# Kernel tuning notes

Hardware: AMD Instinct MI355X
Metric: run time of the kernel (lower is better)

The kernel has to match this reference:

```python
import jax, jax.numpy as jnp
import numpy as np
from jax import lax

W_SIZE = 11
SIGMA = 1.5

def _gaussian_window(w_size, sigma, channel):
    x = np.arange(w_size) - w_size // 2
    g = np.exp(-(x.astype(np.float64) ** 2) / (2.0 * sigma ** 2))
    g = g / g.sum()
    w2d = np.outer(g, g).astype(np.float32)  # [w, w]
    # depthwise kernel in OIHW with feature_group_count=channel: [C, 1, w, w]
    return jnp.asarray(np.broadcast_to(w2d, (channel, 1, w_size, w_size)))

def _dwconv(x, window, channel):
    return lax.conv_general_dilated(
        x, window, window_strides=(1, 1), padding='VALID',
        dimension_numbers=('NCHW', 'OIHW', 'NCHW'),
        feature_group_count=channel)

def setup_inputs() -> dict:
    key = jax.random.key(0)
    k1, k2 = jax.random.split(key)
    B, C, H, W = 16, 3, 512, 512
    y_pred = jax.random.uniform(k1, (B, C, H, W), dtype=jnp.float32)
    y_true = jax.random.uniform(k2, (B, C, H, W), dtype=jnp.float32)
    return {"y_pred": y_pred, "y_true": y_true}

def reference(y_pred, y_true):
    channel = y_pred.shape[1]
    L = jnp.max(y_pred) - jnp.min(y_pred)
    window = _gaussian_window(W_SIZE, SIGMA, channel)

    mu1 = _dwconv(y_pred, window, channel)
    mu2 = _dwconv(y_true, window, channel)
    mu1_sq = mu1 * mu1
    mu2_sq = mu2 * mu2
    mu1_mu2 = mu1 * mu2
    sigma1_sq = _dwconv(y_pred * y_pred, window, channel) - mu1_sq
    sigma2_sq = _dwconv(y_true * y_true, window, channel) - mu2_sq
    sigma12 = _dwconv(y_pred * y_true, window, channel) - mu1_mu2

    C1 = (0.01 * L) ** 2
    C2 = (0.03 * L) ** 2
    v1 = 2.0 * sigma12 + C2
    v2 = sigma1_sq + sigma2_sq + C2
    ssim_map = (2.0 * mu1_mu2 + C1) * v1 / ((mu1_sq + mu2_sq + C1) * v2)
    # size_average=True, full=False defaults
    return -jnp.mean(ssim_map)
```

## Files before the change

### kernel.cpp

```cpp
#include <hip/hip_runtime.h>
#include <math.h>

#define IMG   512
#define OUTD  502
#define NBC   48
#define TH    64
#define TW    32
#define IN_ROWS (TH + 10)
#define SXW   44
#define HBW   32

struct WParams { float w[11]; };


__device__ __forceinline__ unsigned enc_key(float f) {
    unsigned u = __float_as_uint(f);
    return (u & 0x80000000u) ? ~u : (u | 0x80000000u);
}
__device__ __forceinline__ float dec_key(unsigned k) {
    unsigned u = (k & 0x80000000u) ? (k ^ 0x80000000u) : ~k;
    return __uint_as_float(u);
}

__global__ void init_ws(unsigned* wsi, double* wsum) {
    wsi[0] = 0xFFFFFFFFu;
    wsi[1] = 0u;
    wsum[0] = 0.0;
}

__global__ __launch_bounds__(256) void minmax_kernel(const float4* __restrict__ x,
                                                     int n4, unsigned* wsi) {
    float lmin = INFINITY, lmax = -INFINITY;
    for (int i = blockIdx.x * blockDim.x + threadIdx.x; i < n4;
         i += gridDim.x * blockDim.x) {
        float4 v = x[i];
        lmin = fminf(lmin, fminf(fminf(v.x, v.y), fminf(v.z, v.w)));
        lmax = fmaxf(lmax, fmaxf(fmaxf(v.x, v.y), fmaxf(v.z, v.w)));
    }
    for (int o = 32; o; o >>= 1) {
        lmin = fminf(lmin, __shfl_xor(lmin, o));
        lmax = fmaxf(lmax, __shfl_xor(lmax, o));
    }
    __shared__ float smin[4], smax[4];
    int tid = threadIdx.x;
    if ((tid & 63) == 0) { smin[tid >> 6] = lmin; smax[tid >> 6] = lmax; }
    __syncthreads();
    if (tid == 0) {
        float m0 = fminf(fminf(smin[0], smin[1]), fminf(smin[2], smin[3]));
        float m1 = fmaxf(fmaxf(smax[0], smax[1]), fmaxf(smax[2], smax[3]));
        atomicMin(&wsi[0], enc_key(m0));
        atomicMax(&wsi[1], enc_key(m1));
    }
}

__global__ __launch_bounds__(256) void ssim_kernel(const float* __restrict__ x,
                                                   const float* __restrict__ y,
                                                   const unsigned* __restrict__ wsi,
                                                   double* __restrict__ wsum,
                                                   WParams P) {
    __shared__ __align__(16) float sx[IN_ROWS * SXW];
    __shared__ __align__(16) float sy[IN_ROWS * SXW];
    __shared__ __align__(16) float hb[5 * IN_ROWS * HBW];
    __shared__ float wpart[4];

    const int tid = threadIdx.x;
    const int bc  = blockIdx.x;
    const int oy0 = blockIdx.y * TH;
    const int ox0 = blockIdx.z * TW;
    const float* xb = x + (size_t)bc * IMG * IMG;
    const float* yb = y + (size_t)bc * IMG * IMG;

    for (int idx = tid; idx < IN_ROWS * 11; idx += 256) {
        int r = idx / 11, g = idx - r * 11;
        int gy = min(oy0 + r, IMG - 1);
        int gx = min(ox0 + 4 * g, IMG - 4);
        float4 vx = *(const float4*)(xb + gy * IMG + gx);
        float4 vy = *(const float4*)(yb + gy * IMG + gx);
        *(float4*)(sx + r * SXW + 4 * g) = vx;
        *(float4*)(sy + r * SXW + 4 * g) = vy;
    }
    __syncthreads();

    for (int idx = tid; idx < IN_ROWS * 8; idx += 256) {
        int r = idx >> 3, g = idx & 7;
        int c = 4 * g;
        const float* rx = sx + r * SXW + c;
        const float* ry = sy + r * SXW + c;
        float xr[16], yr[16];
        #pragma unroll
        for (int q = 0; q < 4; q++) {
            float4 a = *(const float4*)(rx + 4 * q);
            float4 b = *(const float4*)(ry + 4 * q);
            xr[4*q] = a.x; xr[4*q+1] = a.y; xr[4*q+2] = a.z; xr[4*q+3] = a.w;
            yr[4*q] = b.x; yr[4*q+1] = b.y; yr[4*q+2] = b.z; yr[4*q+3] = b.w;
        }
        float xx[14], yy[14], xy[14];
        #pragma unroll
        for (int e = 0; e < 14; e++) {
            xx[e] = xr[e] * xr[e];
            yy[e] = yr[e] * yr[e];
            xy[e] = xr[e] * yr[e];
        }
        float acc[5][4];
        #pragma unroll
        for (int ch = 0; ch < 5; ch++)
            #pragma unroll
            for (int j = 0; j < 4; j++) acc[ch][j] = 0.f;
        #pragma unroll
        for (int k = 0; k < 11; k++) {
            float w = P.w[k];
            #pragma unroll
            for (int j = 0; j < 4; j++) {
                acc[0][j] += w * xr[j + k];
                acc[1][j] += w * yr[j + k];
                acc[2][j] += w * xx[j + k];
                acc[3][j] += w * yy[j + k];
                acc[4][j] += w * xy[j + k];
            }
        }
        #pragma unroll
        for (int ch = 0; ch < 5; ch++) {
            float4 v = make_float4(acc[ch][0], acc[ch][1], acc[ch][2], acc[ch][3]);
            *(float4*)(hb + (ch * IN_ROWS + r) * HBW + c) = v;
        }
    }

    float fmin_v = dec_key(wsi[0]);
    float fmax_v = dec_key(wsi[1]);
    float L  = fmax_v - fmin_v;
    float C1 = 0.01f * L; C1 *= C1;
    float C2 = 0.03f * L; C2 *= C2;

    __syncthreads();

    const int q  = tid & 15;
    const int rr = tid >> 4;
    const int r0 = 4 * rr;
    const int c  = 2 * q;

    float2 acc[5][4];
    #pragma unroll
    for (int ch = 0; ch < 5; ch++)
        #pragma unroll
        for (int o = 0; o < 4; o++) { acc[ch][o].x = 0.f; acc[ch][o].y = 0.f; }

    #pragma unroll
    for (int k = 0; k < 14; k++) {
        #pragma unroll
        for (int ch = 0; ch < 5; ch++) {
            float2 v = *(const float2*)(hb + (ch * IN_ROWS + r0 + k) * HBW + c);
            #pragma unroll
            for (int o = 0; o < 4; o++) {
                int t = k - o;
                if (t >= 0 && t <= 10) {
                    acc[ch][o].x += P.w[t] * v.x;
                    acc[ch][o].y += P.w[t] * v.y;
                }
            }
        }
    }

    float lsum = 0.f;
    #pragma unroll
    for (int o = 0; o < 4; o++) {
        int oy = oy0 + r0 + o;
        #pragma unroll
        for (int cc = 0; cc < 2; cc++) {
            int ox = ox0 + c + cc;
            if (oy < OUTD && ox < OUTD) {
                float m1  = cc ? acc[0][o].y : acc[0][o].x;
                float m2  = cc ? acc[1][o].y : acc[1][o].x;
                float e11 = cc ? acc[2][o].y : acc[2][o].x;
                float e22 = cc ? acc[3][o].y : acc[3][o].x;
                float e12 = cc ? acc[4][o].y : acc[4][o].x;
                float m1s = m1 * m1, m2s = m2 * m2, m12 = m1 * m2;
                float v1  = 2.f * (e12 - m12) + C2;
                float v2  = (e11 - m1s) + (e22 - m2s) + C2;
                float num = (2.f * m12 + C1) * v1;
                float den = (m1s + m2s + C1) * v2;
                float rc  = __builtin_amdgcn_rcpf(den);
                rc = rc * (2.f - den * rc);
                lsum += num * rc;
            }
        }
    }

    for (int o = 32; o; o >>= 1) lsum += __shfl_xor(lsum, o);
    if ((tid & 63) == 0) wpart[tid >> 6] = lsum;
    __syncthreads();
    if (tid == 0) {
        double t = (double)wpart[0] + (double)wpart[1] +
                   (double)wpart[2] + (double)wpart[3];
        atomicAdd(wsum, t);
    }
}

__global__ void finalize_kernel(const double* wsum, float* out) {
    const double count = (double)NBC * OUTD * OUTD;
    out[0] = (float)(-wsum[0] / count);
}

extern "C" void kernel_launch(void* const* d_in, const int* in_sizes, int n_in,
                              void* d_out, int out_size, void* d_ws, size_t ws_size,
                              hipStream_t stream) {
    (void)n_in; (void)out_size; (void)ws_size;
    const float* y_pred = (const float*)d_in[0];
    const float* y_true = (const float*)d_in[1];
    float* out = (float*)d_out;

    unsigned* wsi = (unsigned*)d_ws;
    double* wsum = (double*)((char*)d_ws + 8);

    WParams P;
    {
        double g[11], s = 0.0;
        for (int i = 0; i < 11; i++) {
            double d = (double)(i - 5);
            g[i] = exp(-(d * d) / (2.0 * 1.5 * 1.5));
            s += g[i];
        }
        for (int i = 0; i < 11; i++) P.w[i] = (float)(g[i] / s);
    }

    init_ws<<<1, 1, 0, stream>>>(wsi, wsum);

    int n4 = in_sizes[0] / 4;
    minmax_kernel<<<2048, 256, 0, stream>>>((const float4*)y_pred, n4, wsi);

    dim3 grid(NBC, (OUTD + TH - 1) / TH, (OUTD + TW - 1) / TW);
    ssim_kernel<<<grid, 256, 0, stream>>>(y_pred, y_true, wsi, wsum, P);

    finalize_kernel<<<1, 1, 0, stream>>>(wsum, out);
}
```

Baseline: 249.4 us.

## Read input tiles directly from global memory and fuse finalize via last-block counter

```diff
diff --git a/kernel.cpp b/kernel.cpp
--- a/kernel.cpp
+++ b/kernel.cpp
@@ -7,8 +7,10 @@
 #define TH    64
 #define TW    32
 #define IN_ROWS (TH + 10)
-#define SXW   44
 #define HBW   32
+#define GY    8
+#define GZ    16
+#define TOTAL_BLOCKS (NBC * GY * GZ)
 
 struct WParams { float w[11]; };
 
@@ -20,12 +22,6 @@
 __device__ __forceinline__ float dec_key(unsigned k) {
     unsigned u = (k & 0x80000000u) ? (k ^ 0x80000000u) : ~k;
     return __uint_as_float(u);
-}
-
-__global__ void init_ws(unsigned* wsi, double* wsum) {
-    wsi[0] = 0xFFFFFFFFu;
-    wsi[1] = 0u;
-    wsum[0] = 0.0;
 }
 
 __global__ __launch_bounds__(256) void minmax_kernel(const float4* __restrict__ x,
@@ -53,13 +49,40 @@
     }
 }
 
+template<int J0>
+__device__ __forceinline__ void hconv(const float* __restrict__ w,
+                                      const float xr[16], const float yr[16],
+                                      float acc[5][4]) {
+    float xx[16], yy[16], xy[16];
+    #pragma unroll
+    for (int e = 0; e < 16; e++) {
+        xx[e] = xr[e] * xr[e];
+        yy[e] = yr[e] * yr[e];
+        xy[e] = xr[e] * yr[e];
+    }
+    #pragma unroll
+    for (int k = 0; k < 11; k++) {
+        float wk = w[k];
+        #pragma unroll
+        for (int j = 0; j < 4; j++) {
+            int i = J0 + j + k;
+            if (i > 15) i = 15;
+            acc[0][j] += wk * xr[i];
+            acc[1][j] += wk * yr[i];
+            acc[2][j] += wk * xx[i];
+            acc[3][j] += wk * yy[i];
+            acc[4][j] += wk * xy[i];
+        }
+    }
+}
+
 __global__ __launch_bounds__(256) void ssim_kernel(const float* __restrict__ x,
                                                    const float* __restrict__ y,
                                                    const unsigned* __restrict__ wsi,
                                                    double* __restrict__ wsum,
+                                                   unsigned* __restrict__ wcount,
+                                                   float* __restrict__ out,
                                                    WParams P) {
-    __shared__ __align__(16) float sx[IN_ROWS * SXW];
-    __shared__ __align__(16) float sy[IN_ROWS * SXW];
     __shared__ __align__(16) float hb[5 * IN_ROWS * HBW];
     __shared__ float wpart[4];
 
@@ -70,22 +93,13 @@
     const float* xb = x + (size_t)bc * IMG * IMG;
     const float* yb = y + (size_t)bc * IMG * IMG;
 
-    for (int idx = tid; idx < IN_ROWS * 11; idx += 256) {
-        int r = idx / 11, g = idx - r * 11;
-        int gy = min(oy0 + r, IMG - 1);
-        int gx = min(ox0 + 4 * g, IMG - 4);
-        float4 vx = *(const float4*)(xb + gy * IMG + gx);
-        float4 vy = *(const float4*)(yb + gy * IMG + gx);
-        *(float4*)(sx + r * SXW + 4 * g) = vx;
-        *(float4*)(sy + r * SXW + 4 * g) = vy;
-    }
-    __syncthreads();
-
     for (int idx = tid; idx < IN_ROWS * 8; idx += 256) {
         int r = idx >> 3, g = idx & 7;
-        int c = 4 * g;
-        const float* rx = sx + r * SXW + c;
-        const float* ry = sy + r * SXW + c;
+        int gy   = min(oy0 + r, IMG - 1);
+        int col0 = ox0 + 4 * g;
+        int gx0  = min(col0, IMG - 16);
+        const float* rx = xb + gy * IMG + gx0;
+        const float* ry = yb + gy * IMG + gx0;
         float xr[16], yr[16];
         #pragma unroll
         for (int q = 0; q < 4; q++) {
@@ -94,34 +108,17 @@
             xr[4*q] = a.x; xr[4*q+1] = a.y; xr[4*q+2] = a.z; xr[4*q+3] = a.w;
             yr[4*q] = b.x; yr[4*q+1] = b.y; yr[4*q+2] = b.z; yr[4*q+3] = b.w;
         }
-        float xx[14], yy[14], xy[14];
-        #pragma unroll
-        for (int e = 0; e < 14; e++) {
-            xx[e] = xr[e] * xr[e];
-            yy[e] = yr[e] * yr[e];
-            xy[e] = xr[e] * yr[e];
-        }
         float acc[5][4];
         #pragma unroll
         for (int ch = 0; ch < 5; ch++)
             #pragma unroll
             for (int j = 0; j < 4; j++) acc[ch][j] = 0.f;
-        #pragma unroll
-        for (int k = 0; k < 11; k++) {
-            float w = P.w[k];
-            #pragma unroll
-            for (int j = 0; j < 4; j++) {
-                acc[0][j] += w * xr[j + k];
-                acc[1][j] += w * yr[j + k];
-                acc[2][j] += w * xx[j + k];
-                acc[3][j] += w * yy[j + k];
-                acc[4][j] += w * xy[j + k];
-            }
-        }
+        if (col0 <= IMG - 16) hconv<0>(P.w, xr, yr, acc);
+        else                  hconv<4>(P.w, xr, yr, acc);
         #pragma unroll
         for (int ch = 0; ch < 5; ch++) {
             float4 v = make_float4(acc[ch][0], acc[ch][1], acc[ch][2], acc[ch][3]);
-            *(float4*)(hb + (ch * IN_ROWS + r) * HBW + c) = v;
+            *(float4*)(hb + (ch * IN_ROWS + r) * HBW + 4 * g) = v;
         }
     }
 
@@ -192,12 +189,15 @@
         double t = (double)wpart[0] + (double)wpart[1] +
                    (double)wpart[2] + (double)wpart[3];
         atomicAdd(wsum, t);
-    }
-}
-
-__global__ void finalize_kernel(const double* wsum, float* out) {
-    const double count = (double)NBC * OUTD * OUTD;
-    out[0] = (float)(-wsum[0] / count);
+        __threadfence();
+        unsigned done = atomicAdd(wcount, 1u);
+        if (done == TOTAL_BLOCKS - 1) {
+            __threadfence();
+            double total = atomicAdd(wsum, 0.0);
+            const double count = (double)NBC * OUTD * OUTD;
+            out[0] = (float)(-total / count);
+        }
+    }
 }
 
 extern "C" void kernel_launch(void* const* d_in, const int* in_sizes, int n_in,
@@ -208,8 +208,9 @@
     const float* y_true = (const float*)d_in[1];
     float* out = (float*)d_out;
 
-    unsigned* wsi = (unsigned*)d_ws;
-    double* wsum = (double*)((char*)d_ws + 8);
+    unsigned* wsi    = (unsigned*)d_ws;
+    double*   wsum   = (double*)((char*)d_ws + 8);
+    unsigned* wcount = (unsigned*)((char*)d_ws + 16);
 
     WParams P;
     {
@@ -222,13 +223,12 @@
         for (int i = 0; i < 11; i++) P.w[i] = (float)(g[i] / s);
     }
 
-    init_ws<<<1, 1, 0, stream>>>(wsi, wsum);
+    hipMemsetAsync(d_ws, 0xFF, 4, stream);
+    hipMemsetAsync((char*)d_ws + 4, 0, 16, stream);
 
     int n4 = in_sizes[0] / 4;
     minmax_kernel<<<2048, 256, 0, stream>>>((const float4*)y_pred, n4, wsi);
 
-    dim3 grid(NBC, (OUTD + TH - 1) / TH, (OUTD + TW - 1) / TW);
-    ssim_kernel<<<grid, 256, 0, stream>>>(y_pred, y_true, wsi, wsum, P);
-
-    finalize_kernel<<<1, 1, 0, stream>>>(wsum, out);
-}
+    dim3 grid(NBC, GY, GZ);
+    ssim_kernel<<<grid, 256, 0, stream>>>(y_pred, y_true, wsi, wsum, wcount, out, P);
+}
```

Result: slower. 381.6 us (+53.0%).

## Double SSIM block threads, fold finalize into last block, memset workspace

Applied to the files above, without the earlier changes.

```diff
diff --git a/kernel.cpp b/kernel.cpp
--- a/kernel.cpp
+++ b/kernel.cpp
@@ -9,6 +9,10 @@
 #define IN_ROWS (TH + 10)
 #define SXW   44
 #define HBW   32
+#define NT    512
+#define GY    8
+#define GZ    16
+#define TOTAL_BLOCKS (NBC * GY * GZ)
 
 struct WParams { float w[11]; };
 
@@ -20,12 +24,6 @@
 __device__ __forceinline__ float dec_key(unsigned k) {
     unsigned u = (k & 0x80000000u) ? (k ^ 0x80000000u) : ~k;
     return __uint_as_float(u);
-}
-
-__global__ void init_ws(unsigned* wsi, double* wsum) {
-    wsi[0] = 0xFFFFFFFFu;
-    wsi[1] = 0u;
-    wsum[0] = 0.0;
 }
 
 __global__ __launch_bounds__(256) void minmax_kernel(const float4* __restrict__ x,
@@ -53,15 +51,17 @@
     }
 }
 
-__global__ __launch_bounds__(256) void ssim_kernel(const float* __restrict__ x,
-                                                   const float* __restrict__ y,
-                                                   const unsigned* __restrict__ wsi,
-                                                   double* __restrict__ wsum,
-                                                   WParams P) {
+__global__ __launch_bounds__(NT, 4) void ssim_kernel(const float* __restrict__ x,
+                                                     const float* __restrict__ y,
+                                                     const unsigned* __restrict__ wsi,
+                                                     double* __restrict__ wsum,
+                                                     unsigned* __restrict__ wcount,
+                                                     float* __restrict__ out,
+                                                     WParams P) {
     __shared__ __align__(16) float sx[IN_ROWS * SXW];
     __shared__ __align__(16) float sy[IN_ROWS * SXW];
     __shared__ __align__(16) float hb[5 * IN_ROWS * HBW];
-    __shared__ float wpart[4];
+    __shared__ float wpart[8];
 
     const int tid = threadIdx.x;
     const int bc  = blockIdx.x;
@@ -70,7 +70,7 @@
     const float* xb = x + (size_t)bc * IMG * IMG;
     const float* yb = y + (size_t)bc * IMG * IMG;
 
-    for (int idx = tid; idx < IN_ROWS * 11; idx += 256) {
+    for (int idx = tid; idx < IN_ROWS * 11; idx += NT) {
         int r = idx / 11, g = idx - r * 11;
         int gy = min(oy0 + r, IMG - 1);
         int gx = min(ox0 + 4 * g, IMG - 4);
@@ -81,7 +81,7 @@
     }
     __syncthreads();
 
-    for (int idx = tid; idx < IN_ROWS * 8; idx += 256) {
+    for (int idx = tid; idx < IN_ROWS * 8; idx += NT) {
         int r = idx >> 3, g = idx & 7;
         int c = 4 * g;
         const float* rx = sx + r * SXW + c;
@@ -133,55 +133,48 @@
 
     __syncthreads();
 
-    const int q  = tid & 15;
-    const int rr = tid >> 4;
-    const int r0 = 4 * rr;
-    const int c  = 2 * q;
-
-    float2 acc[5][4];
+    const int col = tid & 31;
+    const int r0  = 4 * (tid >> 5);
+    const float* hbase = hb + r0 * HBW + col;
+
+    float acc[5][4];
     #pragma unroll
     for (int ch = 0; ch < 5; ch++)
         #pragma unroll
-        for (int o = 0; o < 4; o++) { acc[ch][o].x = 0.f; acc[ch][o].y = 0.f; }
+        for (int o = 0; o < 4; o++) acc[ch][o] = 0.f;
 
     #pragma unroll
     for (int k = 0; k < 14; k++) {
         #pragma unroll
         for (int ch = 0; ch < 5; ch++) {
-            float2 v = *(const float2*)(hb + (ch * IN_ROWS + r0 + k) * HBW + c);
+            float v = hbase[(ch * IN_ROWS + k) * HBW];
             #pragma unroll
             for (int o = 0; o < 4; o++) {
                 int t = k - o;
-                if (t >= 0 && t <= 10) {
-                    acc[ch][o].x += P.w[t] * v.x;
-                    acc[ch][o].y += P.w[t] * v.y;
-                }
+                if (t >= 0 && t <= 10) acc[ch][o] += P.w[t] * v;
             }
         }
     }
 
     float lsum = 0.f;
+    const int ox = ox0 + col;
     #pragma unroll
     for (int o = 0; o < 4; o++) {
         int oy = oy0 + r0 + o;
-        #pragma unroll
-        for (int cc = 0; cc < 2; cc++) {
-            int ox = ox0 + c + cc;
-            if (oy < OUTD && ox < OUTD) {
-                float m1  = cc ? acc[0][o].y : acc[0][o].x;
-                float m2  = cc ? acc[1][o].y : acc[1][o].x;
-                float e11 = cc ? acc[2][o].y : acc[2][o].x;
-                float e22 = cc ? acc[3][o].y : acc[3][o].x;
-                float e12 = cc ? acc[4][o].y : acc[4][o].x;
-                float m1s = m1 * m1, m2s = m2 * m2, m12 = m1 * m2;
-                float v1  = 2.f * (e12 - m12) + C2;
-                float v2  = (e11 - m1s) + (e22 - m2s) + C2;
-                float num = (2.f * m12 + C1) * v1;
-                float den = (m1s + m2s + C1) * v2;
-                float rc  = __builtin_amdgcn_rcpf(den);
-                rc = rc * (2.f - den * rc);
-                lsum += num * rc;
-            }
+        if (oy < OUTD && ox < OUTD) {
+            float m1  = acc[0][o];
+            float m2  = acc[1][o];
+            float e11 = acc[2][o];
+            float e22 = acc[3][o];
+            float e12 = acc[4][o];
+            float m1s = m1 * m1, m2s = m2 * m2, m12 = m1 * m2;
+            float v1  = 2.f * (e12 - m12) + C2;
+            float v2  = (e11 - m1s) + (e22 - m2s) + C2;
+            float num = (2.f * m12 + C1) * v1;
+            float den = (m1s + m2s + C1) * v2;
+            float rc  = __builtin_amdgcn_rcpf(den);
+            rc = rc * (2.f - den * rc);
+            lsum += num * rc;
         }
     }
 
@@ -189,15 +182,19 @@
     if ((tid & 63) == 0) wpart[tid >> 6] = lsum;
     __syncthreads();
     if (tid == 0) {
-        double t = (double)wpart[0] + (double)wpart[1] +
-                   (double)wpart[2] + (double)wpart[3];
+        double t = 0.0;
+        #pragma unroll
+        for (int wv = 0; wv < 8; wv++) t += (double)wpart[wv];
         atomicAdd(wsum, t);
-    }
-}
-
-__global__ void finalize_kernel(const double* wsum, float* out) {
-    const double count = (double)NBC * OUTD * OUTD;
-    out[0] = (float)(-wsum[0] / count);
+        __threadfence();
+        unsigned done = atomicAdd(wcount, 1u);
+        if (done == TOTAL_BLOCKS - 1) {
+            __threadfence();
+            double total = atomicAdd(wsum, 0.0);
+            const double count = (double)NBC * OUTD * OUTD;
+            out[0] = (float)(-total / count);
+        }
+    }
 }
 
 extern "C" void kernel_launch(void* const* d_in, const int* in_sizes, int n_in,
@@ -208,8 +205,9 @@
     const float* y_true = (const float*)d_in[1];
     float* out = (float*)d_out;
 
-    unsigned* wsi = (unsigned*)d_ws;
-    double* wsum = (double*)((char*)d_ws + 8);
+    unsigned* wsi    = (unsigned*)d_ws;
+    double*   wsum   = (double*)((char*)d_ws + 8);
+    unsigned* wcount = (unsigned*)((char*)d_ws + 16);
 
     WParams P;
     {
@@ -222,13 +220,12 @@
         for (int i = 0; i < 11; i++) P.w[i] = (float)(g[i] / s);
     }
 
-    init_ws<<<1, 1, 0, stream>>>(wsi, wsum);
+    hipMemsetAsync(d_ws, 0xFF, 4, stream);
+    hipMemsetAsync((char*)d_ws + 4, 0, 16, stream);
 
     int n4 = in_sizes[0] / 4;
     minmax_kernel<<<2048, 256, 0, stream>>>((const float4*)y_pred, n4, wsi);
 
-    dim3 grid(NBC, (OUTD + TH - 1) / TH, (OUTD + TW - 1) / TW);
-    ssim_kernel<<<grid, 256, 0, stream>>>(y_pred, y_true, wsi, wsum, P);
-
-    finalize_kernel<<<1, 1, 0, stream>>>(wsum, out);
-}
+    dim3 grid(NBC, GY, GZ);
+    ssim_kernel<<<grid, NT, 0, stream>>>(y_pred, y_true, wsi, wsum, wcount, out, P);
+}
```

Result: slower. 388.1 us (+55.6%).
